# Kernel tuning notes

Hardware: AMD Instinct MI355X
Metric: run time of the kernel (lower is better)

The kernel has to match this reference:

```python
import jax, jax.numpy as jnp
import numpy as np

B, L, H = 4, 200, 225   # batch, seq_len, hidden (=15*15)
V = 221                 # input_dim + 1 (padding_idx=0)
EPS = 1e-5


def _bn(x, g, b):
    # training-mode batchnorm over (N, spatial), channel axis = 1
    red = (0,) + tuple(range(2, x.ndim))
    m = jnp.mean(x, red, keepdims=True)
    v = jnp.var(x, red, keepdims=True)
    shp = [1] * x.ndim
    shp[1] = -1
    return (x - m) / jnp.sqrt(v + EPS) * g.reshape(shp) + b.reshape(shp)


def _conv3(x, w, sd):
    return jax.lax.conv_general_dilated(
        x, w, (sd, 1, 1), [(1, 1)] * 3,
        dimension_numbers=('NCDHW', 'OIDHW', 'NCDHW'))


def _conv2(x, w):
    return jax.lax.conv_general_dilated(
        x, w, (1, 1), [(1, 1)] * 2,
        dimension_numbers=('NCHW', 'OIHW', 'NCHW'))


def setup_inputs():
    key = jax.random.key(0)
    ks = jax.random.split(key, 16)

    def he(k, shape, fan_in):
        return jax.random.normal(k, shape, jnp.float32) * (2.0 / fan_in) ** 0.5

    emb = he(ks[0], (V, H), H).at[0].set(0.0)  # padding_idx=0 row zeroed
    w3a = he(ks[1], (4, 1, 3, 3, 3), 1 * 27)
    w3b = he(ks[2], (8, 4, 3, 3, 3), 4 * 27)
    w3c = he(ks[3], (4, 8, 3, 3, 3), 8 * 27)
    w3d = he(ks[4], (1, 4, 3, 3, 3), 4 * 27)
    w2 = he(ks[5], (5, 25, 25, 3, 3), 25 * 9)  # 5 residual conv2d blocks
    fc1_w = he(ks[6], (200, 450), 450)
    fc1_b = jnp.zeros((200,), jnp.float32)
    fc2_w = he(ks[7], (1, 200), 200)
    fc2_b = jnp.zeros((1,), jnp.float32)
    x = jax.random.randint(ks[8], (B, L), 0, V)
    return dict(
        x=x, emb=emb,
        w3a=w3a, g3a=jnp.ones(4), b3a=jnp.zeros(4),
        w3b=w3b, g3b=jnp.ones(8), b3b=jnp.zeros(8),
        w3c=w3c, g3c=jnp.ones(4), b3c=jnp.zeros(4),
        w3d=w3d, g3d=jnp.ones(1), b3d=jnp.zeros(1),
        w2=w2, g2=jnp.ones((5, 25)), b2=jnp.zeros((5, 25)),
        fc1_w=fc1_w, fc1_b=fc1_b, fc2_w=fc2_w, fc2_b=fc2_b)


def reference(x, emb, w3a, g3a, b3a, w3b, g3b, b3b, w3c, g3c, b3c,
              w3d, g3d, b3d, w2, g2, b2, fc1_w, fc1_b, fc2_w, fc2_b):
    e = emb[x]                                  # [B,L,225]
    img = e.reshape(B, L, 15, 15)
    # vectorized replacement of python double-loop causal mask/pad construction:
    # c3d[b,i,t] = img[b,t] if t <= i else 0
    mask = jnp.tril(jnp.ones((L, L), e.dtype))
    c3d = (img[:, None] * mask[None, :, :, None, None]).reshape(B * L, 1, L, 15, 15)

    h = jax.nn.relu(_bn(_conv3(c3d, w3a, 1), g3a, b3a))   # [N,4,200,15,15]
    h = jax.nn.relu(_bn(_conv3(h, w3b, 2), g3b, b3b))     # [N,8,100,15,15]
    h = jax.nn.relu(_bn(_conv3(h, w3c, 2), g3c, b3c))     # [N,4,50,15,15]
    h = jax.nn.relu(_bn(_conv3(h, w3d, 2), g3d, b3d))     # [N,1,25,15,15]

    z = h[:, 0]                                 # squeeze -> [N,25,15,15]
    for i in range(5):
        z = z + jax.nn.relu(_bn(_conv2(z, w2[i]), g2[i], b2[i]))

    # AdaptiveAvgPool3d((1,15,15)) on [N,1,25,15,15] == mean over depth 25
    pooled = jnp.mean(z, axis=1).reshape(B * L, 225)
    feat = jnp.concatenate([pooled, e.reshape(B * L, 225)], axis=1)  # [N,450]
    hfc = jnp.tanh(feat @ fc1_w.T + fc1_b)
    return jax.nn.sigmoid(hfc @ fc2_w.T + fc2_b)  # [N,1]
```

## Files before the change

kernel.cpp:

```cpp
#include <hip/hip_runtime.h>
#include <math.h>

#define DEV __device__ __forceinline__

constexpr int B = 4, L = 200, SP = 225;
constexpr int C1 = 4, D1 = 200;
constexpr int C2N = 8, D2 = 100;
constexpr int C3N = 4, D3 = 50;
constexpr int D4 = 25;
constexpr float EPS = 1e-5f;

constexpr size_t OFF_F1  = 0;
constexpr size_t OFF_E2  = OFF_F1  + 720000;
constexpr size_t OFF_E1  = OFF_E2  + 720000;
constexpr size_t OFF_SS1 = OFF_E1  + 720000;
constexpr size_t OFF_PAR = OFF_SS1 + 19200;
constexpr size_t OFF_F2  = OFF_PAR + 1024;
constexpr size_t OFF_C2  = OFF_F2  + 720000;
constexpr size_t OFF_T2  = OFF_C2  + 1800;
constexpr size_t OFF_SS2F= OFF_T2  + 2880000;
constexpr size_t OFF_SS2T= OFF_SS2F+ 6400;
constexpr size_t OFF_SS2C= OFF_SS2T+ 51200;
constexpr size_t OFF_F3  = OFF_SS2C+ 16;
constexpr size_t OFF_C3  = OFF_F3  + 180000;
constexpr size_t OFF_T3  = OFF_C3  + 900;
constexpr size_t OFF_SS3F= OFF_T3  + 1440000;
constexpr size_t OFF_SS3T= OFF_SS3F+ 1600;
constexpr size_t OFF_SS3C= OFF_SS3T+ 12800;
constexpr size_t OFF_F4  = OFF_SS3C+ 8;
constexpr size_t OFF_C4  = OFF_F4  + 22500;
constexpr size_t OFF_T4  = OFF_C4  + 225;
constexpr size_t OFF_SS4F= OFF_T4  + 360000;
constexpr size_t OFF_SS4T= OFF_SS4F+ 200;
constexpr size_t OFF_SS4C= OFF_SS4T+ 3200;
constexpr size_t OFF_Z   = OFF_SS4C+ 2;
constexpr size_t OFF_CB  = OFF_Z   + 4500000;
constexpr size_t OFF_P2D = OFF_CB  + 4500000;
constexpr size_t WS_FLOATS = OFF_P2D + 40000;


DEV float waveRed(float v) {
    #pragma unroll
    for (int m = 32; m; m >>= 1) v += __shfl_xor(v, m, 64);
    return v;
}
DEV double blockSumD(double v, double* red) {
    int tid = threadIdx.x;
    red[tid] = v; __syncthreads();
    for (int s = 128; s > 0; s >>= 1) { if (tid < s) red[tid] += red[tid + s]; __syncthreads(); }
    double r = red[0]; __syncthreads(); return r;
}
DEV float conv9(const float* S, const float* w, int y, int x) {
    float a = 0.f;
    for (int ky = 0; ky < 3; ky++) { int yy = y + ky - 1; if (yy < 0 || yy >= 15) continue;
        for (int kx = 0; kx < 3; kx++) { int xx = x + kx - 1; if (xx < 0 || xx >= 15) continue;
            a += w[ky * 3 + kx] * S[yy * 15 + xx]; } }
    return a;
}
DEV void gather9(const float* Sp, int y, int x, float* s9) {
    #pragma unroll
    for (int ky = 0; ky < 3; ky++) {
        int yy = y + ky - 1; bool oky = (yy >= 0 && yy < 15);
        #pragma unroll
        for (int kx = 0; kx < 3; kx++) {
            int xx = x + kx - 1; bool ok = oky && (xx >= 0 && xx < 15);
            s9[ky * 3 + kx] = ok ? Sp[yy * 15 + xx] : 0.f;
        }
    }
}

__global__ __launch_bounds__(256) void k_layer1(const int* __restrict__ xi, const float* __restrict__ emb,
                        const float* __restrict__ w3a, float* F1, float* E2, float* E1, float* SS1) {
    __shared__ float simg[675];
    __shared__ float wl[108];
    __shared__ float red[96];
    int blk = blockIdx.x;
    int d = blk % D1; int b = blk / D1;
    int tid = threadIdx.x;
    if (tid < 108) wl[tid] = w3a[tid];
    for (int idx = tid; idx < 675; idx += 256) {
        int t = idx / 225, pos = idx % 225;
        int j = d + t - 1; float v = 0.f;
        if (j >= 0 && j < L) v = emb[(size_t)xi[b * L + j] * SP + pos];
        simg[idx] = v;
    }
    __syncthreads();
    int y = tid / 15, x = tid % 15;
    int w = tid >> 6;
    #pragma unroll 1
    for (int c = 0; c < 4; c++) {
        float f1 = 0.f, e2 = 0.f, e1 = 0.f;
        if (tid < 225) {
            float P0 = conv9(simg,       wl + c * 27,      y, x);
            float P1 = conv9(simg + 225, wl + c * 27 + 9,  y, x);
            float P2 = conv9(simg + 450, wl + c * 27 + 18, y, x);
            f1 = P0 + P1 + P2; e2 = P0 + P1; e1 = P0;
            size_t o = ((size_t)(b * C1 + c) * D1 + d) * SP + tid;
            F1[o] = f1; E2[o] = e2; E1[o] = e1;
        }
        float r0 = waveRed(f1), r1 = waveRed(f1 * f1), r2 = waveRed(e2),
              r3 = waveRed(e2 * e2), r4 = waveRed(e1), r5 = waveRed(e1 * e1);
        if ((tid & 63) == 0) {
            float* rp = red + w * 24 + c * 6;
            rp[0] = r0; rp[1] = r1; rp[2] = r2; rp[3] = r3; rp[4] = r4; rp[5] = r5;
        }
    }
    __syncthreads();
    if (tid < 24) {
        float s = red[tid] + red[24 + tid] + red[48 + tid] + red[72 + tid];
        int c = tid / 6, q = tid % 6;
        SS1[q * 3200 + (b * C1 + c) * D1 + d] = s;
    }
}

__global__ void k_stats1(const float* SS1, const float* g, const float* bb, float* par) {
    __shared__ double dred[256];
    int c = blockIdx.x; int tid = threadIdx.x;
    double s = 0, q = 0;
    for (int idx = tid; idx < B * D1; idx += 256) {
        int b = idx / D1, d = idx % D1;
        int sl = (b * C1 + c) * D1 + d;
        double wF = (double)(L - 1 - d);
        s += wF * SS1[sl] + SS1[6400 + sl] + (d >= 1 ? SS1[12800 + sl] : 0.0);
        q += wF * SS1[3200 + sl] + SS1[9600 + sl] + (d >= 1 ? SS1[16000 + sl] : 0.0);
    }
    s = blockSumD(s, dred); q = blockSumD(q, dred);
    if (tid == 0) {
        double N = (double)B * L * D1 * SP;
        double mean = s / N, var = q / N - mean * mean;
        float sc = g[c] / (float)sqrt(var + (double)EPS);
        float sh = bb[c] - (float)mean * sc;
        par[c] = sc; par[4 + c] = sh; par[8 + c] = fmaxf(sh, 0.f);
    }
}

__global__ __launch_bounds__(256) void k_F2(const float* __restrict__ F1raw, const float* __restrict__ par,
                        const float* __restrict__ w3b, float* F2, float* SS2F) {
    __shared__ float S[2700];
    __shared__ float wl[108];
    __shared__ float red[8];
    int blk = blockIdx.x; int d2 = blk % D2; int c2 = (blk / D2) % C2N; int b = blk / (D2 * C2N);
    int tid = threadIdx.x;
    if (tid < 108) wl[tid] = w3b[c2 * 108 + tid];
    for (int idx = tid; idx < 2700; idx += 256) {
        int p = idx / 225, pos = idx % 225; int t = p >> 2, c = p & 3;
        int j = 2 * d2 - 1 + t; float v = 0.f;
        if (j >= 0 && j < D1)
            v = fmaxf(par[c] * F1raw[((size_t)(b * C1 + c) * D1 + j) * SP + pos] + par[4 + c], 0.f);
        S[idx] = v;
    }
    __syncthreads();
    float acc = 0.f;
    if (tid < 225) {
        int y = tid / 15, x = tid % 15;
        #pragma unroll 1
        for (int t = 0; t < 3; t++)
            for (int c = 0; c < 4; c++)
                acc += conv9(S + (t * 4 + c) * 225, wl + c * 27 + t * 9, y, x);
        F2[(size_t)blk * SP + tid] = acc;
    }
    float sm = waveRed(acc), sq = waveRed(acc * acc);
    if ((tid & 63) == 0) { red[(tid >> 6) * 2] = sm; red[(tid >> 6) * 2 + 1] = sq; }
    __syncthreads();
    if (tid == 0) { SS2F[blk] = red[0] + red[2] + red[4] + red[6]; SS2F[3200 + blk] = red[1] + red[3] + red[5] + red[7]; }
}

__global__ void k_C2(const float* __restrict__ par, const float* __restrict__ w3b, float* C2b, float* SS2C) {
    __shared__ float red[64];
    int tid = threadIdx.x; int y = tid / 15, x = tid % 15; int w = tid >> 6;
    #pragma unroll 1
    for (int c2 = 0; c2 < C2N; c2++) {
        float acc = 0.f;
        if (tid < 225) {
            for (int c = 0; c < C1; c++) {
                float z1 = par[8 + c];
                for (int t = 0; t < 3; t++) {
                    float ws = 0.f;
                    for (int ky = 0; ky < 3; ky++) { int yy = y + ky - 1; if (yy < 0 || yy >= 15) continue;
                        for (int kx = 0; kx < 3; kx++) { int xx = x + kx - 1; if (xx < 0 || xx >= 15) continue;
                            ws += w3b[c2 * 108 + c * 27 + t * 9 + ky * 3 + kx]; } }
                    acc += z1 * ws;
                }
            }
            C2b[c2 * SP + tid] = acc;
        }
        float sm = waveRed(acc), sq = waveRed(acc * acc);
        if ((tid & 63) == 0) { red[w * 16 + c2 * 2] = sm; red[w * 16 + c2 * 2 + 1] = sq; }
    }
    __syncthreads();
    if (tid < 16) SS2C[tid] = red[tid] + red[16 + tid] + red[32 + tid] + red[48 + tid];
}

__global__ __launch_bounds__(256) void k_T2(const float* __restrict__ F1raw, const float* __restrict__ E2raw,
                    const float* __restrict__ E1raw, const float* __restrict__ par,
                    const float* __restrict__ w3b, float* T2, float* SS2T) {
    __shared__ float S[4500];
    __shared__ float wl[864];
    __shared__ float red[64];
    int blk = blockIdx.x; int i = blk % L, b = blk / L; int tid = threadIdx.x;
    int t2a = i >> 1, jbase = 2 * t2a - 1;
    for (int k = tid; k < 864; k += 256) wl[k] = w3b[k];
    for (int idx = tid; idx < 4500; idx += 256) {
        int p = idx / 225, pos = idx % 225; int sl = p >> 2, c = p & 3;
        int j = jbase + sl; float v = 0.f;
        if (j >= 0 && j < L) {
            if (j <= i - 1)      v = fmaxf(par[c] * F1raw[((size_t)(b * C1 + c) * D1 + j) * SP + pos] + par[4 + c], 0.f);
            else if (j == i)     v = fmaxf(par[c] * E2raw[((size_t)(b * C1 + c) * D1 + j) * SP + pos] + par[4 + c], 0.f);
            else if (j == i + 1) v = fmaxf(par[c] * E1raw[((size_t)(b * C1 + c) * D1 + j) * SP + pos] + par[4 + c], 0.f);
            else                 v = par[8 + c];
        }
        S[idx] = v;
    }
    __syncthreads();
    int y = tid / 15, x = tid % 15;
    #pragma unroll 1
    for (int k = 0; k < 2; k++) {
        float vals[8] = {0,0,0,0,0,0,0,0};
        int d2 = t2a + k;
        if (d2 < D2 && tid < 225) {
            #pragma unroll 1
            for (int t = 0; t < 3; t++) {
                int sl = 2 * k + t;
                #pragma unroll 1
                for (int c = 0; c < 4; c++) {
                    float s9[9];
                    gather9(S + (sl * 4 + c) * 225, y, x, s9);
                    const float* wb = wl + c * 27 + t * 9;
                    #pragma unroll
                    for (int c2 = 0; c2 < 8; c2++) {
                        const float* wc = wb + c2 * 108;
                        float a = 0.f;
                        #pragma unroll
                        for (int q = 0; q < 9; q++) a += wc[q] * s9[q];
                        vals[c2] += a;
                    }
                }
            }
        }
        if (tid < 225)
            #pragma unroll
            for (int c2 = 0; c2 < 8; c2++) T2[(((size_t)blk * 2 + k) * C2N + c2) * SP + tid] = vals[c2];
        #pragma unroll
        for (int c2 = 0; c2 < 8; c2++) {
            float sm = waveRed(vals[c2]), sq = waveRed(vals[c2] * vals[c2]);
            if ((tid & 63) == 0) { red[(tid >> 6) * 16 + c2 * 2] = sm; red[(tid >> 6) * 16 + c2 * 2 + 1] = sq; }
        }
        __syncthreads();
        if (tid < 16) {
            float s = red[tid] + red[16 + tid] + red[32 + tid] + red[48 + tid];
            int c2 = tid >> 1, q = tid & 1;
            (q ? SS2T + 25600 : SS2T)[((size_t)blk * 2 + k) * C2N + c2] = s;
        }
        __syncthreads();
    }
}

__global__ void k_stats2(const float* SS2F, const float* SS2T, const float* SS2C,
                         const float* g, const float* bb, float* par) {
    __shared__ double dred[256];
    int c2 = blockIdx.x; int tid = threadIdx.x;
    double s = 0, q = 0;
    for (int idx = tid; idx < B * D2; idx += 256) {
        int d2 = idx % D2; int b = idx / D2;
        int wv = L - 2 * d2 - 2; if (wv < 0) wv = 0;
        int sl = (b * C2N + c2) * D2 + d2;
        s += (double)wv * SS2F[sl]; q += (double)wv * SS2F[3200 + sl];
    }
    for (int idx = tid; idx < B * L * 2; idx += 256) {
        int sl = idx * C2N + c2;
        s += SS2T[sl]; q += SS2T[25600 + sl];
    }
    {
        int cnt = 0;
        for (int i = tid; i < L; i += 256) { int v = D2 - (i >> 1) - 2; if (v > 0) cnt += v; }
        double wv = (double)cnt * B;
        s += wv * SS2C[c2 * 2]; q += wv * SS2C[c2 * 2 + 1];
    }
    s = blockSumD(s, dred); q = blockSumD(q, dred);
    if (tid == 0) {
        double N = (double)B * L * D2 * SP;
        double mean = s / N, var = q / N - mean * mean;
        float sc = g[c2] / (float)sqrt(var + (double)EPS);
        float sh = bb[c2] - (float)mean * sc;
        par[16 + c2] = sc; par[24 + c2] = sh;
    }
}

__global__ __launch_bounds__(256) void k_F3(const float* __restrict__ F2raw, const float* __restrict__ par,
                        const float* __restrict__ w3c, float* F3, float* SS3F) {
    __shared__ float S[5400];
    __shared__ float wl[216];
    __shared__ float red[8];
    int blk = blockIdx.x; int d3 = blk % D3; int c3 = (blk / D3) % C3N; int b = blk / (D3 * C3N);
    int tid = threadIdx.x;
    if (tid < 216) wl[tid] = w3c[c3 * 216 + tid];
    for (int idx = tid; idx < 5400; idx += 256) {
        int p = idx / 225, pos = idx % 225; int t = p >> 3, c2 = p & 7;
        int j2 = 2 * d3 - 1 + t; float v = 0.f;
        if (j2 >= 0 && j2 < D2)
            v = fmaxf(par[16 + c2] * F2raw[((size_t)(b * C2N + c2) * D2 + j2) * SP + pos] + par[24 + c2], 0.f);
        S[idx] = v;
    }
    __syncthreads();
    float acc = 0.f;
    if (tid < 225) {
        int y = tid / 15, x = tid % 15;
        #pragma unroll 1
        for (int t = 0; t < 3; t++)
            for (int c2 = 0; c2 < 8; c2++)
                acc += conv9(S + (t * 8 + c2) * 225, wl + c2 * 27 + t * 9, y, x);
        F3[(size_t)blk * SP + tid] = acc;
    }
    float sm = waveRed(acc), sq = waveRed(acc * acc);
    if ((tid & 63) == 0) { red[(tid >> 6) * 2] = sm; red[(tid >> 6) * 2 + 1] = sq; }
    __syncthreads();
    if (tid == 0) { SS3F[blk] = red[0] + red[2] + red[4] + red[6]; SS3F[800 + blk] = red[1] + red[3] + red[5] + red[7]; }
}

__global__ void k_C3(const float* __restrict__ C2braw, const float* __restrict__ par,
                     const float* __restrict__ w3c, float* C3b, float* SS3C) {
    __shared__ float S[1800];
    __shared__ float red[32];
    int tid = threadIdx.x; int w = tid >> 6;
    for (int idx = tid; idx < 1800; idx += 256) {
        int c2 = idx / 225;
        S[idx] = fmaxf(par[16 + c2] * C2braw[idx] + par[24 + c2], 0.f);
    }
    __syncthreads();
    int y = tid / 15, x = tid % 15;
    #pragma unroll 1
    for (int c3 = 0; c3 < C3N; c3++) {
        float acc = 0.f;
        if (tid < 225) {
            for (int t = 0; t < 3; t++)
                for (int c2 = 0; c2 < C2N; c2++)
                    acc += conv9(S + c2 * 225, w3c + c3 * 216 + c2 * 27 + t * 9, y, x);
            C3b[c3 * SP + tid] = acc;
        }
        float sm = waveRed(acc), sq = waveRed(acc * acc);
        if ((tid & 63) == 0) { red[w * 8 + c3 * 2] = sm; red[w * 8 + c3 * 2 + 1] = sq; }
    }
    __syncthreads();
    if (tid < 8) SS3C[tid] = red[tid] + red[8 + tid] + red[16 + tid] + red[24 + tid];
}

__global__ __launch_bounds__(256) void k_T3(const float* __restrict__ F2raw, const float* __restrict__ T2raw,
                    const float* __restrict__ C2braw, const float* __restrict__ par,
                    const float* __restrict__ w3c, float* T3, float* SS3T) {
    __shared__ float S[9000];
    __shared__ float wl[864];
    __shared__ float red[32];
    int blk = blockIdx.x; int i = blk % L, b = blk / L; int tid = threadIdx.x;
    int t2a = i >> 1, t3a = i >> 2, j2base = 2 * t3a - 1;
    for (int k = tid; k < 864; k += 256) wl[k] = w3c[k];
    for (int idx = tid; idx < 9000; idx += 256) {
        int p = idx / 225, pos = idx % 225; int sl = p >> 3, c2 = p & 7;
        int j2 = j2base + sl; float v = 0.f;
        if (j2 >= 0 && j2 < D2) {
            float raw;
            if (j2 < t2a)           raw = F2raw[((size_t)(b * C2N + c2) * D2 + j2) * SP + pos];
            else if (j2 == t2a)     raw = T2raw[(((size_t)blk * 2 + 0) * C2N + c2) * SP + pos];
            else if (j2 == t2a + 1) raw = T2raw[(((size_t)blk * 2 + 1) * C2N + c2) * SP + pos];
            else                    raw = C2braw[c2 * SP + pos];
            v = fmaxf(par[16 + c2] * raw + par[24 + c2], 0.f);
        }
        S[idx] = v;
    }
    __syncthreads();
    int y = tid / 15, x = tid % 15;
    #pragma unroll 1
    for (int k = 0; k < 2; k++) {
        float vals[4] = {0, 0, 0, 0};
        int d3 = t3a + k;
        if (d3 < D3 && tid < 225) {
            #pragma unroll 1
            for (int t = 0; t < 3; t++) {
                int sl = 2 * k + t;
                #pragma unroll 1
                for (int c2 = 0; c2 < 8; c2++) {
                    float s9[9];
                    gather9(S + (sl * 8 + c2) * 225, y, x, s9);
                    const float* wb = wl + c2 * 27 + t * 9;
                    #pragma unroll
                    for (int c3 = 0; c3 < 4; c3++) {
                        const float* wc = wb + c3 * 216;
                        float a = 0.f;
                        #pragma unroll
                        for (int q = 0; q < 9; q++) a += wc[q] * s9[q];
                        vals[c3] += a;
                    }
                }
            }
        }
        if (tid < 225)
            #pragma unroll
            for (int c3 = 0; c3 < 4; c3++) T3[(((size_t)blk * 2 + k) * C3N + c3) * SP + tid] = vals[c3];
        #pragma unroll
        for (int c3 = 0; c3 < 4; c3++) {
            float sm = waveRed(vals[c3]), sq = waveRed(vals[c3] * vals[c3]);
            if ((tid & 63) == 0) { red[(tid >> 6) * 8 + c3 * 2] = sm; red[(tid >> 6) * 8 + c3 * 2 + 1] = sq; }
        }
        __syncthreads();
        if (tid < 8) {
            float s = red[tid] + red[8 + tid] + red[16 + tid] + red[24 + tid];
            int c3 = tid >> 1, q = tid & 1;
            (q ? SS3T + 6400 : SS3T)[((size_t)blk * 2 + k) * C3N + c3] = s;
        }
        __syncthreads();
    }
}

__global__ void k_stats3(const float* SS3F, const float* SS3T, const float* SS3C,
                         const float* g, const float* bb, float* par) {
    __shared__ double dred[256];
    int c3 = blockIdx.x; int tid = threadIdx.x;
    double s = 0, q = 0;
    for (int idx = tid; idx < B * D3; idx += 256) {
        int d3 = idx % D3; int b = idx / D3;
        int wv = L - 4 * d3 - 4; if (wv < 0) wv = 0;
        int sl = (b * C3N + c3) * D3 + d3;
        s += (double)wv * SS3F[sl]; q += (double)wv * SS3F[800 + sl];
    }
    for (int idx = tid; idx < B * L * 2; idx += 256) {
        int sl = idx * C3N + c3;
        s += SS3T[sl]; q += SS3T[6400 + sl];
    }
    {
        int cnt = 0;
        for (int i = tid; i < L; i += 256) { int v = D3 - (i >> 2) - 2; if (v > 0) cnt += v; }
        double wv = (double)cnt * B;
        s += wv * SS3C[c3 * 2]; q += wv * SS3C[c3 * 2 + 1];
    }
    s = blockSumD(s, dred); q = blockSumD(q, dred);
    if (tid == 0) {
        double N = (double)B * L * D3 * SP;
        double mean = s / N, var = q / N - mean * mean;
        float sc = g[c3] / (float)sqrt(var + (double)EPS);
        float sh = bb[c3] - (float)mean * sc;
        par[32 + c3] = sc; par[36 + c3] = sh;
    }
}

__global__ __launch_bounds__(256) void k_F4(const float* __restrict__ F3raw, const float* __restrict__ par,
                        const float* __restrict__ w3d, float* F4, float* SS4F) {
    __shared__ float S[2700];
    __shared__ float wl[108];
    __shared__ float red[8];
    int blk = blockIdx.x; int d4 = blk % D4; int b = blk / D4; int tid = threadIdx.x;
    if (tid < 108) wl[tid] = w3d[tid];
    for (int idx = tid; idx < 2700; idx += 256) {
        int p = idx / 225, pos = idx % 225; int t = p >> 2, c3 = p & 3;
        int j3 = 2 * d4 - 1 + t; float v = 0.f;
        if (j3 >= 0 && j3 < D3)
            v = fmaxf(par[32 + c3] * F3raw[((size_t)(b * C3N + c3) * D3 + j3) * SP + pos] + par[36 + c3], 0.f);
        S[idx] = v;
    }
    __syncthreads();
    float acc = 0.f;
    if (tid < 225) {
        int y = tid / 15, x = tid % 15;
        #pragma unroll 1
        for (int t = 0; t < 3; t++)
            for (int c3 = 0; c3 < 4; c3++)
                acc += conv9(S + (t * 4 + c3) * 225, wl + c3 * 27 + t * 9, y, x);
        F4[(size_t)blk * SP + tid] = acc;
    }
    float sm = waveRed(acc), sq = waveRed(acc * acc);
    if ((tid & 63) == 0) { red[(tid >> 6) * 2] = sm; red[(tid >> 6) * 2 + 1] = sq; }
    __syncthreads();
    if (tid == 0) { SS4F[blk] = red[0] + red[2] + red[4] + red[6]; SS4F[100 + blk] = red[1] + red[3] + red[5] + red[7]; }
}

__global__ void k_C4(const float* __restrict__ C3braw, const float* __restrict__ par,
                     const float* __restrict__ w3d, float* C4b, float* SS4C) {
    __shared__ float S[900];
    __shared__ float red[8];
    int tid = threadIdx.x;
    for (int idx = tid; idx < 900; idx += 256) {
        int c3 = idx / 225;
        S[idx] = fmaxf(par[32 + c3] * C3braw[idx] + par[36 + c3], 0.f);
    }
    __syncthreads();
    int y = tid / 15, x = tid % 15;
    float acc = 0.f;
    if (tid < 225) {
        for (int t = 0; t < 3; t++)
            for (int c3 = 0; c3 < C3N; c3++)
                acc += conv9(S + c3 * 225, w3d + c3 * 27 + t * 9, y, x);
        C4b[tid] = acc;
    }
    float sm = waveRed(acc), sq = waveRed(acc * acc);
    if ((tid & 63) == 0) { red[(tid >> 6) * 2] = sm; red[(tid >> 6) * 2 + 1] = sq; }
    __syncthreads();
    if (tid == 0) { SS4C[0] = red[0] + red[2] + red[4] + red[6]; SS4C[1] = red[1] + red[3] + red[5] + red[7]; }
}

__global__ __launch_bounds__(256) void k_T4(const float* __restrict__ F3raw, const float* __restrict__ T3raw,
                    const float* __restrict__ C3braw, const float* __restrict__ par,
                    const float* __restrict__ w3d, float* T4, float* SS4T) {
    __shared__ float S[4500];
    __shared__ float wl[108];
    __shared__ float red[8];
    int blk = blockIdx.x; int i = blk % L, b = blk / L; int tid = threadIdx.x;
    int t3a = i >> 2, t4a = i >> 3, j3base = 2 * t4a - 1;
    if (tid < 108) wl[tid] = w3d[tid];
    for (int idx = tid; idx < 4500; idx += 256) {
        int p = idx / 225, pos = idx % 225; int sl = p >> 2, c3 = p & 3;
        int j3 = j3base + sl; float v = 0.f;
        if (j3 >= 0 && j3 < D3) {
            float raw;
            if (j3 < t3a)           raw = F3raw[((size_t)(b * C3N + c3) * D3 + j3) * SP + pos];
            else if (j3 == t3a)     raw = T3raw[(((size_t)blk * 2 + 0) * C3N + c3) * SP + pos];
            else if (j3 == t3a + 1) raw = T3raw[(((size_t)blk * 2 + 1) * C3N + c3) * SP + pos];
            else                    raw = C3braw[c3 * SP + pos];
            v = fmaxf(par[32 + c3] * raw + par[36 + c3], 0.f);
        }
        S[idx] = v;
    }
    __syncthreads();
    int y = tid / 15, x = tid % 15;
    #pragma unroll 1
    for (int k = 0; k < 2; k++) {
        float acc = 0.f;
        int d4 = t4a + k;
        if (d4 < D4 && tid < 225) {
            #pragma unroll 1
            for (int t = 0; t < 3; t++) {
                int sl = 2 * k + t;
                #pragma unroll 1
                for (int c3 = 0; c3 < 4; c3++) {
                    float s9[9];
                    gather9(S + (sl * 4 + c3) * 225, y, x, s9);
                    const float* wc = wl + c3 * 27 + t * 9;
                    float a = 0.f;
                    #pragma unroll
                    for (int q = 0; q < 9; q++) a += wc[q] * s9[q];
                    acc += a;
                }
            }
        }
        if (tid < 225) T4[((size_t)blk * 2 + k) * SP + tid] = acc;
        float sm = waveRed(acc), sq = waveRed(acc * acc);
        if ((tid & 63) == 0) { red[(tid >> 6) * 2] = sm; red[(tid >> 6) * 2 + 1] = sq; }
        __syncthreads();
        if (tid == 0) {
            SS4T[blk * 2 + k] = red[0] + red[2] + red[4] + red[6];
            SS4T[1600 + blk * 2 + k] = red[1] + red[3] + red[5] + red[7];
        }
        __syncthreads();
    }
}

__global__ void k_stats4(const float* SS4F, const float* SS4T, const float* SS4C,
                         const float* g, const float* bb, float* par) {
    __shared__ double dred[256];
    int tid = threadIdx.x; double s = 0, q = 0;
    for (int idx = tid; idx < B * D4; idx += 256) {
        int d4 = idx % D4; int b = idx / D4;
        int wv = L - 8 * d4 - 8; if (wv < 0) wv = 0;
        s += (double)wv * SS4F[b * D4 + d4]; q += (double)wv * SS4F[100 + b * D4 + d4];
    }
    for (int idx = tid; idx < B * L * 2; idx += 256) {
        s += SS4T[idx]; q += SS4T[1600 + idx];
    }
    {
        int cnt = 0;
        for (int i = tid; i < L; i += 256) { int v = D4 - (i >> 3) - 2; if (v > 0) cnt += v; }
        double wv = (double)cnt * B;
        s += wv * SS4C[0]; q += wv * SS4C[1];
    }
    s = blockSumD(s, dred); q = blockSumD(q, dred);
    if (tid == 0) {
        double N = (double)B * L * D4 * SP;
        double mean = s / N, var = q / N - mean * mean;
        float sc = g[0] / (float)sqrt(var + (double)EPS);
        float sh = bb[0] - (float)mean * sc;
        par[40] = sc; par[41] = sh;
    }
}

__global__ void k_trfc1(const float* __restrict__ fc1w, float* __restrict__ fc1T) {
    int idx = blockIdx.x * 256 + threadIdx.x;
    if (idx >= 200 * 450) return;
    int o = idx % 200, k = idx / 200;
    fc1T[idx] = fc1w[(size_t)o * 450 + k];
}

template<int MODE>
__global__ __launch_bounds__(384) void k_conv2d(const float* __restrict__ zin, float* __restrict__ zout,
        const float* __restrict__ cprev, const float* __restrict__ par,
        const float* __restrict__ F4s, const float* __restrict__ T4s, const float* __restrict__ C4s,
        const float* __restrict__ w2it, float* __restrict__ cbuf, float* __restrict__ part) {
    __shared__ float zs[5625];
    __shared__ float wl[5625];
    __shared__ float rowsum[375], rowsq[375];
    int s = blockIdx.x, tid = threadIdx.x;
    int i = s % L, b = s / L; int t4a = i >> 3;
    for (int k = tid; k < 5625; k += 384) wl[k] = w2it[k];
    for (int idx = tid; idx < 5625; idx += 384) {
        int c = idx / 225, pos = idx % 225;
        float v;
        if (MODE == 0) {
            float raw;
            if (c < t4a)           raw = F4s[((size_t)b * D4 + c) * SP + pos];
            else if (c == t4a)     raw = T4s[((size_t)s * 2 + 0) * SP + pos];
            else if (c == t4a + 1) raw = T4s[((size_t)s * 2 + 1) * SP + pos];
            else                   raw = C4s[pos];
            v = fmaxf(par[40] * raw + par[41], 0.f);
        } else {
            v = zin[(size_t)s * 5625 + idx] + fmaxf(par[48 + c] * cprev[(size_t)s * 5625 + idx] + par[80 + c], 0.f);
        }
        zout[(size_t)s * 5625 + idx] = v;
        zs[idx] = v;
    }
    __syncthreads();
    if (tid < 375) {
        int c2 = tid / 15, y = tid % 15;
        float acc[15];
        #pragma unroll
        for (int xx = 0; xx < 15; xx++) acc[xx] = 0.f;
        const float* wrow = wl + c2 * 225;
        #pragma unroll 1
        for (int c = 0; c < 25; c++) {
            const float* wcc = wrow + c * 9;
            #pragma unroll
            for (int ky = 0; ky < 3; ky++) {
                int yy = y + ky - 1; if (yy < 0 || yy >= 15) continue;
                const float* zr = zs + c * 225 + yy * 15;
                float w0 = wcc[ky * 3 + 0], w1 = wcc[ky * 3 + 1], w2v = wcc[ky * 3 + 2];
                float rv[15];
                #pragma unroll
                for (int xx = 0; xx < 15; xx++) rv[xx] = zr[xx];
                acc[0] += w1 * rv[0] + w2v * rv[1];
                #pragma unroll
                for (int xx = 1; xx < 14; xx++) acc[xx] += w0 * rv[xx - 1] + w1 * rv[xx] + w2v * rv[xx + 1];
                acc[14] += w0 * rv[13] + w1 * rv[14];
            }
        }
        float sm = 0.f, sq = 0.f;
        #pragma unroll
        for (int xx = 0; xx < 15; xx++) {
            float v = acc[xx]; sm += v; sq += v * v;
            cbuf[(size_t)s * 5625 + tid * 15 + xx] = v;
        }
        rowsum[tid] = sm; rowsq[tid] = sq;
    }
    __syncthreads();
    if (tid < 25) {
        float sm = 0.f, sq = 0.f;
        for (int r = tid * 15; r < tid * 15 + 15; r++) { sm += rowsum[r]; sq += rowsq[r]; }
        part[((size_t)s * 25 + tid) * 2] = sm; part[((size_t)s * 25 + tid) * 2 + 1] = sq;
    }
}

__global__ void k_stats2d(const float* part, const float* g, const float* bb, float* par) {
    __shared__ double dred[256];
    int c = blockIdx.x, tid = threadIdx.x;
    double s = 0, q = 0;
    for (int ss = tid; ss < B * L; ss += 256) { s += part[((size_t)ss * 25 + c) * 2]; q += part[((size_t)ss * 25 + c) * 2 + 1]; }
    s = blockSumD(s, dred); q = blockSumD(q, dred);
    if (tid == 0) {
        double N = (double)B * L * SP;
        double mean = s / N, var = q / N - mean * mean;
        float sc = g[c] / (float)sqrt(var + (double)EPS);
        float sh = bb[c] - (float)mean * sc;
        par[48 + c] = sc; par[80 + c] = sh;
    }
}

__global__ __launch_bounds__(256) void k_head(const float* __restrict__ z, const float* __restrict__ cbuf,
                      const float* __restrict__ par, const int* __restrict__ xi, const float* __restrict__ emb,
                      const float* __restrict__ fc1T, const float* __restrict__ fc1b,
                      const float* __restrict__ fc2w, const float* __restrict__ fc2b,
                      float* __restrict__ out) {
    __shared__ float feat[450];
    __shared__ float red[4];
    int s = blockIdx.x, tid = threadIdx.x;
    if (tid < 225) {
        float sm = 0.f;
        for (int c = 0; c < 25; c++) {
            size_t o = (size_t)s * 5625 + c * 225 + tid;
            sm += z[o] + fmaxf(par[48 + c] * cbuf[o] + par[80 + c], 0.f);
        }
        feat[tid] = sm * (1.f / 25.f);
        feat[225 + tid] = emb[(size_t)xi[s] * SP + tid];
    }
    __syncthreads();
    float hv = 0.f;
    {
        float acc = (tid < 200) ? fc1b[tid] : 0.f;
        for (int k = 0; k < 450; k++) {
            float wv = (tid < 200) ? fc1T[k * 200 + tid] : 0.f;
            acc += feat[k] * wv;
        }
        if (tid < 200) hv = tanhf(acc) * fc2w[tid];
    }
    float tot = waveRed(hv);
    if ((tid & 63) == 0) red[tid >> 6] = tot;
    __syncthreads();
    if (tid == 0) out[s] = 1.f / (1.f + expf(-(red[0] + red[1] + red[2] + red[3] + fc2b[0])));
}

extern "C" void kernel_launch(void* const* d_in, const int* in_sizes, int n_in,
                              void* d_out, int out_size, void* d_ws, size_t ws_size,
                              hipStream_t stream) {
    const int*   xi   = (const int*)d_in[0];
    const float* emb  = (const float*)d_in[1];
    const float* w3a  = (const float*)d_in[2];
    const float* g3a  = (const float*)d_in[3];
    const float* b3a  = (const float*)d_in[4];
    const float* w3b  = (const float*)d_in[5];
    const float* g3b  = (const float*)d_in[6];
    const float* b3b  = (const float*)d_in[7];
    const float* w3c  = (const float*)d_in[8];
    const float* g3c  = (const float*)d_in[9];
    const float* b3c  = (const float*)d_in[10];
    const float* w3d  = (const float*)d_in[11];
    const float* g3d  = (const float*)d_in[12];
    const float* b3d  = (const float*)d_in[13];
    const float* w2   = (const float*)d_in[14];
    const float* g2   = (const float*)d_in[15];
    const float* b2   = (const float*)d_in[16];
    const float* fc1w = (const float*)d_in[17];
    const float* fc1b = (const float*)d_in[18];
    const float* fc2w = (const float*)d_in[19];
    const float* fc2b = (const float*)d_in[20];
    float* ws = (float*)d_ws;
    float* out = (float*)d_out;
    if (ws_size < WS_FLOATS * sizeof(float)) return;

    float* F1  = ws + OFF_F1;   float* E2  = ws + OFF_E2;  float* E1  = ws + OFF_E1;
    float* SS1 = ws + OFF_SS1;  float* par = ws + OFF_PAR;
    float* F2  = ws + OFF_F2;   float* C2b = ws + OFF_C2;  float* T2  = ws + OFF_T2;
    float* SS2F= ws + OFF_SS2F; float* SS2T= ws + OFF_SS2T; float* SS2C= ws + OFF_SS2C;
    float* F3  = ws + OFF_F3;   float* C3b = ws + OFF_C3;  float* T3  = ws + OFF_T3;
    float* SS3F= ws + OFF_SS3F; float* SS3T= ws + OFF_SS3T; float* SS3C= ws + OFF_SS3C;
    float* F4  = ws + OFF_F4;   float* C4b = ws + OFF_C4;  float* T4  = ws + OFF_T4;
    float* SS4F= ws + OFF_SS4F; float* SS4T= ws + OFF_SS4T; float* SS4C= ws + OFF_SS4C;
    float* z   = ws + OFF_Z;    float* cb  = ws + OFF_CB;  float* p2d = ws + OFF_P2D;
    float* fc1T = ws + OFF_E2;

    k_layer1<<<B * D1, 256, 0, stream>>>(xi, emb, w3a, F1, E2, E1, SS1);
    k_stats1<<<4, 256, 0, stream>>>(SS1, g3a, b3a, par);
    k_F2<<<B * C2N * D2, 256, 0, stream>>>(F1, par, w3b, F2, SS2F);
    k_C2<<<1, 256, 0, stream>>>(par, w3b, C2b, SS2C);
    k_T2<<<B * L, 256, 0, stream>>>(F1, E2, E1, par, w3b, T2, SS2T);
    k_trfc1<<<(90000 + 255) / 256, 256, 0, stream>>>(fc1w, fc1T);
    k_stats2<<<8, 256, 0, stream>>>(SS2F, SS2T, SS2C, g3b, b3b, par);
    k_F3<<<B * C3N * D3, 256, 0, stream>>>(F2, par, w3c, F3, SS3F);
    k_C3<<<1, 256, 0, stream>>>(C2b, par, w3c, C3b, SS3C);
    k_T3<<<B * L, 256, 0, stream>>>(F2, T2, C2b, par, w3c, T3, SS3T);
    k_stats3<<<4, 256, 0, stream>>>(SS3F, SS3T, SS3C, g3c, b3c, par);
    k_F4<<<B * D4, 256, 0, stream>>>(F3, par, w3d, F4, SS4F);
    k_C4<<<1, 256, 0, stream>>>(C3b, par, w3d, C4b, SS4C);
    k_T4<<<B * L, 256, 0, stream>>>(F3, T3, C3b, par, w3d, T4, SS4T);
    k_stats4<<<1, 256, 0, stream>>>(SS4F, SS4T, SS4C, g3d, b3d, par);

    k_conv2d<0><<<B * L, 384, 0, stream>>>(z, z, cb, par, F4, T4, C4b, w2, cb, p2d);
    k_stats2d<<<25, 256, 0, stream>>>(p2d, g2, b2, par);
    for (int it = 1; it < 5; it++) {
        k_conv2d<1><<<B * L, 384, 0, stream>>>(z, z, cb, par, F4, T4, C4b, w2 + (size_t)it * 5625, cb, p2d);
        k_stats2d<<<25, 256, 0, stream>>>(p2d, g2 + it * 25, b2 + it * 25, par);
    }
    k_head<<<B * L, 256, 0, stream>>>(z, cb, par, xi, emb, fc1T, fc1b, fc2w, fc2b, out);
}
```

Before: 684.1 us.

## Restructure conv2d to one pixel per thread with all output channels in registers

The 2D residual conv kernel now assigns one spatial pixel per thread and accumulates all 25 output channels in registers. Each thread gathers a 3x3 input neighbourhood once per input channel, and the weights are read directly from global memory as uniform loads instead of being staged in shared memory. Per-channel sum and sum-of-squares are reduced with wave reductions. This cuts shared-memory traffic and the block size, at the cost of more registers per thread and 31 idle lanes out of 256.

```diff
diff --git a/kernel.cpp b/kernel.cpp
--- a/kernel.cpp
+++ b/kernel.cpp
@@ -587,17 +587,15 @@
 }
 
 template<int MODE>
-__global__ __launch_bounds__(384) void k_conv2d(const float* __restrict__ zin, float* __restrict__ zout,
+__global__ __launch_bounds__(256) void k_conv2d(const float* __restrict__ zin, float* __restrict__ zout,
         const float* __restrict__ cprev, const float* __restrict__ par,
         const float* __restrict__ F4s, const float* __restrict__ T4s, const float* __restrict__ C4s,
         const float* __restrict__ w2it, float* __restrict__ cbuf, float* __restrict__ part) {
     __shared__ float zs[5625];
-    __shared__ float wl[5625];
-    __shared__ float rowsum[375], rowsq[375];
+    __shared__ float red[200];
     int s = blockIdx.x, tid = threadIdx.x;
     int i = s % L, b = s / L; int t4a = i >> 3;
-    for (int k = tid; k < 5625; k += 384) wl[k] = w2it[k];
-    for (int idx = tid; idx < 5625; idx += 384) {
+    for (int idx = tid; idx < 5625; idx += 256) {
         int c = idx / 225, pos = idx % 225;
         float v;
         if (MODE == 0) {
@@ -614,50 +612,43 @@
         zs[idx] = v;
     }
     __syncthreads();
-    if (tid < 375) {
-        int c2 = tid / 15, y = tid % 15;
-        float acc[15];
+    float acc[25];
+    #pragma unroll
+    for (int c2 = 0; c2 < 25; c2++) acc[c2] = 0.f;
+    bool act = tid < 225;
+    int y = act ? tid / 15 : 0, x = act ? tid % 15 : 0;
+    #pragma unroll 1
+    for (int c = 0; c < 25; c++) {
+        float s9[9];
+        gather9(zs + c * 225, y, x, s9);
+        const float* wc = w2it + c * 9;
         #pragma unroll
-        for (int xx = 0; xx < 15; xx++) acc[xx] = 0.f;
-        const float* wrow = wl + c2 * 225;
-        #pragma unroll 1
-        for (int c = 0; c < 25; c++) {
-            const float* wcc = wrow + c * 9;
+        for (int c2 = 0; c2 < 25; c2++) {
+            const float* w9 = wc + c2 * 225;
+            float a = 0.f;
             #pragma unroll
-            for (int ky = 0; ky < 3; ky++) {
-                int yy = y + ky - 1; if (yy < 0 || yy >= 15) continue;
-                const float* zr = zs + c * 225 + yy * 15;
-                float w0 = wcc[ky * 3 + 0], w1 = wcc[ky * 3 + 1], w2v = wcc[ky * 3 + 2];
-                float rv[15];
-                #pragma unroll
-                for (int xx = 0; xx < 15; xx++) rv[xx] = zr[xx];
-                acc[0] += w1 * rv[0] + w2v * rv[1];
-                #pragma unroll
-                for (int xx = 1; xx < 14; xx++) acc[xx] += w0 * rv[xx - 1] + w1 * rv[xx] + w2v * rv[xx + 1];
-                acc[14] += w0 * rv[13] + w1 * rv[14];
-            }
-        }
-        float sm = 0.f, sq = 0.f;
-        #pragma unroll
-        for (int xx = 0; xx < 15; xx++) {
-            float v = acc[xx]; sm += v; sq += v * v;
-            cbuf[(size_t)s * 5625 + tid * 15 + xx] = v;
-        }
-        rowsum[tid] = sm; rowsq[tid] = sq;
-    }
-    __syncthreads();
-    if (tid < 25) {
-        float sm = 0.f, sq = 0.f;
-        for (int r = tid * 15; r < tid * 15 + 15; r++) { sm += rowsum[r]; sq += rowsq[r]; }
-        part[((size_t)s * 25 + tid) * 2] = sm; part[((size_t)s * 25 + tid) * 2 + 1] = sq;
-    }
+            for (int q = 0; q < 9; q++) a += w9[q] * s9[q];
+            acc[c2] += a;
+        }
+    }
+    int w = tid >> 6;
+    #pragma unroll
+    for (int c2 = 0; c2 < 25; c2++) {
+        float v = act ? acc[c2] : 0.f;
+        if (act) cbuf[(size_t)s * 5625 + c2 * 225 + tid] = v;
+        float sm = waveRed(v), sq = waveRed(v * v);
+        if ((tid & 63) == 0) { red[w * 50 + c2 * 2] = sm; red[w * 50 + c2 * 2 + 1] = sq; }
+    }
+    __syncthreads();
+    if (tid < 50)
+        part[(size_t)s * 50 + tid] = red[tid] + red[50 + tid] + red[100 + tid] + red[150 + tid];
 }
 
 __global__ void k_stats2d(const float* part, const float* g, const float* bb, float* par) {
     __shared__ double dred[256];
     int c = blockIdx.x, tid = threadIdx.x;
     double s = 0, q = 0;
-    for (int ss = tid; ss < B * L; ss += 256) { s += part[((size_t)ss * 25 + c) * 2]; q += part[((size_t)ss * 25 + c) * 2 + 1]; }
+    for (int ss = tid; ss < B * L; ss += 256) { s += part[(size_t)ss * 50 + c * 2]; q += part[(size_t)ss * 50 + c * 2 + 1]; }
     s = blockSumD(s, dred); q = blockSumD(q, dred);
     if (tid == 0) {
         double N = (double)B * L * SP;
@@ -756,10 +747,10 @@
     k_T4<<<B * L, 256, 0, stream>>>(F3, T3, C3b, par, w3d, T4, SS4T);
     k_stats4<<<1, 256, 0, stream>>>(SS4F, SS4T, SS4C, g3d, b3d, par);
 
-    k_conv2d<0><<<B * L, 384, 0, stream>>>(z, z, cb, par, F4, T4, C4b, w2, cb, p2d);
+    k_conv2d<0><<<B * L, 256, 0, stream>>>(z, z, cb, par, F4, T4, C4b, w2, cb, p2d);
     k_stats2d<<<25, 256, 0, stream>>>(p2d, g2, b2, par);
     for (int it = 1; it < 5; it++) {
-        k_conv2d<1><<<B * L, 384, 0, stream>>>(z, z, cb, par, F4, T4, C4b, w2 + (size_t)it * 5625, cb, p2d);
+        k_conv2d<1><<<B * L, 256, 0, stream>>>(z, z, cb, par, F4, T4, C4b, w2 + (size_t)it * 5625, cb, p2d);
         k_stats2d<<<25, 256, 0, stream>>>(p2d, g2 + it * 25, b2 + it * 25, par);
     }
     k_head<<<B * L, 256, 0, stream>>>(z, cb, par, xi, emb, fc1T, fc1b, fc2w, fc2b, out);
```

Measured after the change: 745.9 us. 9.0% more time.
